# Kernel optimization log

Measured on AMD Instinct MI355X. Metric: run time of the kernel, lower is better.

Reference implementation:

```python
import jax, jax.numpy as jnp
import numpy as np

D_MODEL = 1024
NUM_HEADS = 16
HEAD_DIM = D_MODEL // NUM_HEADS


def setup_inputs() -> dict:
    key = jax.random.key(0)
    ks = jax.random.split(key, 11)
    N, S = 4, 2048
    s = 1.0 / np.sqrt(D_MODEL)
    return {
        "query": jax.random.normal(ks[0], (N, S, D_MODEL), jnp.float32),
        "key": jax.random.normal(ks[1], (N, S, D_MODEL), jnp.float32),
        "value": jax.random.normal(ks[2], (N, S, D_MODEL), jnp.float32),
        "Wq": jax.random.normal(ks[3], (D_MODEL, D_MODEL), jnp.float32) * s,
        "bq": jnp.zeros((D_MODEL,), jnp.float32),
        "Wk": jax.random.normal(ks[4], (D_MODEL, D_MODEL), jnp.float32) * s,
        "bk": jnp.zeros((D_MODEL,), jnp.float32),
        "Wv": jax.random.normal(ks[5], (D_MODEL, D_MODEL), jnp.float32) * s,
        "bv": jnp.zeros((D_MODEL,), jnp.float32),
        "Wo": jax.random.normal(ks[6], (D_MODEL, D_MODEL), jnp.float32) * s,
        "bo": jnp.zeros((D_MODEL,), jnp.float32),
    }


def reference(query, key, value, Wq, bq, Wk, bk, Wv, bv, Wo, bo):
    N, Q, _ = query.shape
    K = key.shape[1]
    # torch Linear: x @ W^T + b
    q = (query @ Wq.T + bq).reshape(N, Q, NUM_HEADS, HEAD_DIM)
    k = (key @ Wk.T + bk).reshape(N, K, NUM_HEADS, HEAD_DIM)
    v = (value @ Wv.T + bv).reshape(N, K, NUM_HEADS, HEAD_DIM)
    # NOTE: original module applies NO 1/sqrt(head_dim) scaling.
    scores = jnp.einsum('nqhd,nkhd->nhqk', q, k)
    attn = jax.nn.softmax(scores, axis=3)
    out = jnp.einsum('nhqk,nkhd->nqhd', attn, v).reshape(N, Q, D_MODEL)
    return out @ Wo.T + bo
```

## Files before the change

kernel.cpp:

```cpp
#include <hip/hip_runtime.h>
#include <stdint.h>

#define SEQ 2048
#define MROWS 8192
#define LOG2E 1.44269504f

typedef __attribute__((ext_vector_type(8))) _Float16 f16x8;
typedef __attribute__((ext_vector_type(2))) __fp16 fp16x2_t;
typedef __attribute__((ext_vector_type(8))) unsigned short ushort8;
typedef __attribute__((ext_vector_type(4))) unsigned short ushort4_t;
typedef __attribute__((ext_vector_type(4))) float f32x4;
typedef __attribute__((ext_vector_type(16))) float f32x16;

__device__ __forceinline__ unsigned short f32_to_f16u(float f) {
  union { _Float16 h; unsigned short u; } v; v.h = (_Float16)f; return v.u;
}

__device__ __forceinline__ unsigned int pk_u32(float a, float b) {
  union { fp16x2_t h; unsigned int u; } v;
  v.h = __builtin_amdgcn_cvt_pkrtz(a, b);
  return v.u;
}

__device__ __forceinline__ ushort8 pack8_rtz(float4 f0, float4 f1) {
  union { fp16x2_t h2[4]; ushort8 u8; } pk;
  pk.h2[0] = __builtin_amdgcn_cvt_pkrtz(f0.x, f0.y);
  pk.h2[1] = __builtin_amdgcn_cvt_pkrtz(f0.z, f0.w);
  pk.h2[2] = __builtin_amdgcn_cvt_pkrtz(f1.x, f1.y);
  pk.h2[3] = __builtin_amdgcn_cvt_pkrtz(f1.z, f1.w);
  return pk.u8;
}

__device__ __forceinline__ void gload16(const void* g, void* l) {
  __builtin_amdgcn_global_load_lds(
      (const __attribute__((address_space(1))) unsigned int*)g,
      (__attribute__((address_space(3))) unsigned int*)l, 16, 0, 0);
}

__global__ __launch_bounds__(256) void wconv_k(
    const float* __restrict__ Wq, const float* __restrict__ Wk,
    const float* __restrict__ Wv, const float* __restrict__ Wo,
    unsigned short* __restrict__ WF)
{
  const int plane = blockIdx.y;
  const float* __restrict__ s = (plane==0)? Wq : (plane==1)? Wk : (plane==2)? Wv : Wo;
  size_t off = ((size_t)blockIdx.x*256 + threadIdx.x) * 8;
  float4 f0 = *(const float4*)(s + off);
  float4 f1 = *(const float4*)(s + off + 4);
  *(ushort8*)&WF[(size_t)plane*1048576 + off] = pack8_rtz(f0, f1);
}

__global__ __launch_bounds__(256) void qkv_k(
    const float* __restrict__ Aq, const float* __restrict__ Ak, const float* __restrict__ Av,
    const unsigned short* __restrict__ WF,
    const float* __restrict__ bq, const float* __restrict__ bk, const float* __restrict__ bv,
    unsigned short* __restrict__ Qf, unsigned short* __restrict__ Kf, unsigned short* __restrict__ Vt)
{
  const int z = blockIdx.z;
  const float* __restrict__ A    = (z==0)? Aq : (z==1)? Ak : Av;
  const unsigned short* __restrict__ W = WF + (size_t)z*1048576;
  const float* __restrict__ bias = (z==0)? bq : (z==1)? bk : bv;

  __shared__ unsigned short Ah[128*32];
  __shared__ unsigned short Bh[128*32];

  const int tid  = threadIdx.x;
  const int lane = tid & 63;
  const int w    = tid >> 6;
  const int wm   = w >> 1, wn = w & 1;
  const int row0 = blockIdx.x * 128;
  const int col0 = blockIdx.y * 128;

  f32x4 acc[4][4] = {};

  for (int k0 = 0; k0 < 1024; k0 += 32) {
    __syncthreads();
    #pragma unroll
    for (int j=0;j<2;++j) {
      int r  = w*32 + j*16 + (lane>>2);
      int sl = (lane & 3) ^ ((r>>1)&3);
      gload16(W + (size_t)(col0 + r)*1024 + k0 + sl*8, &Bh[(w*32 + j*16)*32]);
    }
    #pragma unroll
    for (int i = 0; i < 2; ++i) {
      int c = tid + i*256;
      int r = c >> 2, slot = c & 3;
      int lidx = r*32 + ((slot ^ ((r >> 1) & 3))*8);
      const float* ap = A + (size_t)(row0 + r)*1024 + k0 + slot*8;
      float4 f0 = *(const float4*)ap;
      float4 f1 = *(const float4*)(ap + 4);
      *(ushort8*)&Ah[lidx] = pack8_rtz(f0, f1);
    }
    __syncthreads();

    f16x8 a_[4], b_[4];
    const int slotR = lane >> 4;
    #pragma unroll
    for (int m=0;m<4;++m) {
      int r = wm*64 + m*16 + (lane & 15);
      a_[m] = *(const f16x8*)&Ah[r*32 + ((slotR ^ ((r>>1)&3))*8)];
    }
    #pragma unroll
    for (int nn=0;nn<4;++nn) {
      int r = wn*64 + nn*16 + (lane & 15);
      b_[nn] = *(const f16x8*)&Bh[r*32 + ((slotR ^ ((r>>1)&3))*8)];
    }
    #pragma unroll
    for (int m=0;m<4;++m)
      #pragma unroll
      for (int nn=0;nn<4;++nn)
        acc[m][nn] = __builtin_amdgcn_mfma_f32_16x16x32_f16(a_[m], b_[nn], acc[m][nn],0,0,0);
  }

  #pragma unroll
  for (int m=0;m<4;++m) {
    #pragma unroll
    for (int nn=0;nn<4;++nn) {
      int gcol = col0 + wn*64 + nn*16 + (lane & 15);
      float bsv = bias[gcol];
      if (z == 2) {
        int rbase = row0 + wm*64 + m*16 + (lane>>4)*4;
        int nIdx = rbase >> 11, s0 = rbase & 2047;
        ushort4_t pk;
        #pragma unroll
        for (int r2=0;r2<4;++r2) pk[r2] = f32_to_f16u(acc[m][nn][r2] + bsv);
        *(ushort4_t*)&Vt[((size_t)(nIdx*1024 + gcol))*2048 + s0] = pk;
      } else {
        unsigned short* __restrict__ dst = (z==0)? Qf : Kf;
        const float qsc = (z==0)? LOG2E : 1.0f;
        #pragma unroll
        for (int r2=0;r2<4;++r2) {
          int grow = row0 + wm*64 + m*16 + (lane>>4)*4 + r2;
          dst[(size_t)grow*1024 + gcol] = f32_to_f16u((acc[m][nn][r2] + bsv) * qsc);
        }
      }
    }
  }
}

__global__ __launch_bounds__(256) void oproj_k(
    const unsigned short* __restrict__ AO, const unsigned short* __restrict__ W,
    const float* __restrict__ bias, float* __restrict__ out)
{
  __shared__ unsigned short Ah[128*32];
  __shared__ unsigned short Bh[128*32];

  const int tid  = threadIdx.x;
  const int lane = tid & 63;
  const int w    = tid >> 6;
  const int wm   = w >> 1, wn = w & 1;
  const int row0 = blockIdx.x * 128;
  const int col0 = blockIdx.y * 128;

  f32x4 acc[4][4] = {};

  for (int k0 = 0; k0 < 1024; k0 += 32) {
    __syncthreads();
    #pragma unroll
    for (int j=0;j<2;++j) {
      int r  = w*32 + j*16 + (lane>>2);
      int sl = (lane & 3) ^ ((r>>1)&3);
      gload16(AO + (size_t)(row0 + r)*1024 + k0 + sl*8, &Ah[(w*32 + j*16)*32]);
      gload16(W  + (size_t)(col0 + r)*1024 + k0 + sl*8, &Bh[(w*32 + j*16)*32]);
    }
    __syncthreads();

    f16x8 a_[4], b_[4];
    const int slotR = lane >> 4;
    #pragma unroll
    for (int m=0;m<4;++m) {
      int r = wm*64 + m*16 + (lane & 15);
      a_[m] = *(const f16x8*)&Ah[r*32 + ((slotR ^ ((r>>1)&3))*8)];
    }
    #pragma unroll
    for (int nn=0;nn<4;++nn) {
      int r = wn*64 + nn*16 + (lane & 15);
      b_[nn] = *(const f16x8*)&Bh[r*32 + ((slotR ^ ((r>>1)&3))*8)];
    }
    #pragma unroll
    for (int m=0;m<4;++m)
      #pragma unroll
      for (int nn=0;nn<4;++nn)
        acc[m][nn] = __builtin_amdgcn_mfma_f32_16x16x32_f16(a_[m], b_[nn], acc[m][nn],0,0,0);
  }

  #pragma unroll
  for (int m=0;m<4;++m)
    #pragma unroll
    for (int nn=0;nn<4;++nn) {
      int gcol = col0 + wn*64 + nn*16 + (lane & 15);
      float bsv = bias[gcol];
      #pragma unroll
      for (int r2=0;r2<4;++r2) {
        int grow = row0 + wm*64 + m*16 + (lane>>4)*4 + r2;
        out[(size_t)grow*1024 + gcol] = acc[m][nn][r2] + bsv;
      }
    }
}

__global__ __launch_bounds__(256) void attn_k(
  const unsigned short* __restrict__ Qf, const unsigned short* __restrict__ Kf,
  const unsigned short* __restrict__ Vt, unsigned short* __restrict__ AO)
{
  __shared__ unsigned short Ks[2][64*64];
  __shared__ unsigned short Vs[2][64*64];

  const int tid = threadIdx.x, lane = tid & 63, w = tid >> 6;
  const int q = lane & 31, h = lane >> 5;

  const int bid = blockIdx.x;
  const int swz = (bid & 7) * 128 + (bid >> 3);
  const int qt = swz & 15, nh = swz >> 4;
  const int n = nh >> 4, hh = nh & 15;

  f16x8 qf[4];
  {
    int qrow = n*SEQ + qt*128 + w*32 + q;
    #pragma unroll
    for (int t=0;t<4;++t)
      qf[t] = *(const f16x8*)&Qf[(size_t)qrow*1024 + hh*64 + t*16 + h*8];
  }

  f32x16 o[2] = {};
  float mrun = -1e30f, lrun = 0.f;

  const size_t kbase = (size_t)(n*SEQ)*1024 + hh*64;
  const size_t vbase = ((size_t)(n*1024 + hh*64))*SEQ;

  #pragma unroll
  for (int i=0;i<2;++i){
    int c = tid + i*256; int r = c>>3, sl = c&7;
    int lidx = r*64 + ((sl^(r&7))*8);
    *(ushort8*)&Ks[0][lidx] = *(const ushort8*)&Kf[kbase + (size_t)r*1024 + sl*8];
    *(ushort8*)&Vs[0][lidx] = *(const ushort8*)&Vt[vbase + (size_t)r*SEQ + sl*8];
  }
  __syncthreads();

  int cur = 0;
  for (int kt = 0; kt < 32; ++kt) {
    ushort8 kreg[2], vreg[2];
    if (kt < 31) {
      #pragma unroll
      for (int i=0;i<2;++i){
        int c = tid + i*256; int r = c>>3, sl = c&7;
        kreg[i] = *(const ushort8*)&Kf[kbase + (size_t)((kt+1)*64 + r)*1024 + sl*8];
        vreg[i] = *(const ushort8*)&Vt[vbase + (size_t)r*SEQ + (kt+1)*64 + sl*8];
      }
    }

    f32x16 s[2] = {};
    __builtin_amdgcn_s_setprio(1);
    #pragma unroll
    for (int t=0; t<4; ++t) {
      int gr = ((2*t+h) ^ (q&7))*8;
      f16x8 k0 = *(const f16x8*)&Ks[cur][(q     )*64 + gr];
      f16x8 k1 = *(const f16x8*)&Ks[cur][(32 + q)*64 + gr];
      s[0] = __builtin_amdgcn_mfma_f32_32x32x16_f16(k0, qf[t], s[0],0,0,0);
      s[1] = __builtin_amdgcn_mfma_f32_32x32x16_f16(k1, qf[t], s[1],0,0,0);
    }
    __builtin_amdgcn_s_setprio(0);

    float m01 = fmaxf(fmaxf(s[0][0], s[0][1]), fmaxf(s[0][2], s[0][3]));
    float m02 = fmaxf(fmaxf(s[0][4], s[0][5]), fmaxf(s[0][6], s[0][7]));
    float m03 = fmaxf(fmaxf(s[0][8], s[0][9]), fmaxf(s[0][10], s[0][11]));
    float m04 = fmaxf(fmaxf(s[0][12], s[0][13]), fmaxf(s[0][14], s[0][15]));
    float m11 = fmaxf(fmaxf(s[1][0], s[1][1]), fmaxf(s[1][2], s[1][3]));
    float m12 = fmaxf(fmaxf(s[1][4], s[1][5]), fmaxf(s[1][6], s[1][7]));
    float m13 = fmaxf(fmaxf(s[1][8], s[1][9]), fmaxf(s[1][10], s[1][11]));
    float m14 = fmaxf(fmaxf(s[1][12], s[1][13]), fmaxf(s[1][14], s[1][15]));
    float ml = fmaxf(fmaxf(fmaxf(m01,m02), fmaxf(m03,m04)),
                     fmaxf(fmaxf(m11,m12), fmaxf(m13,m14)));
    if (!__all(ml <= mrun + 7.0f)) {
      float m2 = fmaxf(ml, __shfl_xor(ml, 32, 64));
      float mn = fmaxf(mrun, m2);
      float sc = __builtin_amdgcn_exp2f(mrun - mn);
      lrun *= sc;
      mrun = mn;
      #pragma unroll
      for (int dd=0; dd<2; ++dd)
        #pragma unroll
        for (int r=0;r<16;++r) o[dd][r] *= sc;
    }
    {
      float m0 = mrun;
      float rsl = 0.f;
      #pragma unroll
      for (int st=0; st<2; ++st)
        #pragma unroll
        for (int r=0;r<16;++r) {
          float p = __builtin_amdgcn_exp2f(s[st][r] - m0);
          s[st][r] = p; rsl += p;
        }
      lrun += rsl;
    }

    f16x8 pf[4];
    #pragma unroll
    for (int st=0; st<2; ++st)
      #pragma unroll
      for (int s_t=0; s_t<2; ++s_t) {
        unsigned int a0 = pk_u32(s[st][8*s_t+0], s[st][8*s_t+1]);
        unsigned int a1 = pk_u32(s[st][8*s_t+2], s[st][8*s_t+3]);
        unsigned int b0 = pk_u32(s[st][8*s_t+4], s[st][8*s_t+5]);
        unsigned int b1 = pk_u32(s[st][8*s_t+6], s[st][8*s_t+7]);
        asm("v_permlane32_swap_b32 %0, %1" : "+v"(a0), "+v"(b0));
        asm("v_permlane32_swap_b32 %0, %1" : "+v"(a1), "+v"(b1));
        union { unsigned int u[4]; f16x8 v; } pkk;
        pkk.u[0] = a0; pkk.u[1] = a1; pkk.u[2] = b0; pkk.u[3] = b1;
        pf[st*2 + s_t] = pkk.v;
      }

    #pragma unroll
    for (int sg=0; sg<4; ++sg) {
      int gr = ((2*sg+h) ^ (q&7))*8;
      f16x8 v0 = *(const f16x8*)&Vs[cur][(q     )*64 + gr];
      f16x8 v1 = *(const f16x8*)&Vs[cur][(32 + q)*64 + gr];
      __builtin_amdgcn_s_setprio(1);
      o[0] = __builtin_amdgcn_mfma_f32_32x32x16_f16(v0, pf[sg], o[0],0,0,0);
      o[1] = __builtin_amdgcn_mfma_f32_32x32x16_f16(v1, pf[sg], o[1],0,0,0);
      __builtin_amdgcn_s_setprio(0);
    }

    if (kt < 31) {
      #pragma unroll
      for (int i=0;i<2;++i){
        int c = tid + i*256; int r = c>>3, sl = c&7;
        int lidx = r*64 + ((sl^(r&7))*8);
        *(ushort8*)&Ks[cur^1][lidx] = kreg[i];
        *(ushort8*)&Vs[cur^1][lidx] = vreg[i];
      }
    }
    __syncthreads();
    cur ^= 1;
  }

  float rs = lrun + __shfl_xor(lrun, 32, 64);
  float inv = 1.0f / rs;
  int qrow = n*SEQ + qt*128 + w*32 + q;
  #pragma unroll
  for (int dd=0; dd<2; ++dd)
    #pragma unroll
    for (int rq=0; rq<4; ++rq) {
      union { fp16x2_t h2[2]; ushort4_t u4; } pk4;
      pk4.h2[0] = __builtin_amdgcn_cvt_pkrtz(o[dd][4*rq+0]*inv, o[dd][4*rq+1]*inv);
      pk4.h2[1] = __builtin_amdgcn_cvt_pkrtz(o[dd][4*rq+2]*inv, o[dd][4*rq+3]*inv);
      int d0 = dd*32 + 8*rq + 4*h;
      *(ushort4_t*)&AO[(size_t)qrow*1024 + hh*64 + d0] = pk4.u4;
    }
}

extern "C" void kernel_launch(void* const* d_in, const int* in_sizes, int n_in,
                              void* d_out, int out_size, void* d_ws, size_t ws_size,
                              hipStream_t stream)
{
  (void)in_sizes; (void)n_in; (void)out_size; (void)ws_size;
  const float* query = (const float*)d_in[0];
  const float* key   = (const float*)d_in[1];
  const float* value = (const float*)d_in[2];
  const float* Wq = (const float*)d_in[3];
  const float* bq = (const float*)d_in[4];
  const float* Wk = (const float*)d_in[5];
  const float* bk = (const float*)d_in[6];
  const float* Wv = (const float*)d_in[7];
  const float* bv = (const float*)d_in[8];
  const float* Wo = (const float*)d_in[9];
  const float* bo = (const float*)d_in[10];
  float* out = (float*)d_out;

  unsigned short* ws = (unsigned short*)d_ws;
  const size_t PLANE = (size_t)MROWS * 1024;
  unsigned short* Qf = ws;
  unsigned short* Kf = Qf + PLANE;
  unsigned short* Vt = Kf + PLANE;
  unsigned short* AO = Vt + PLANE;
  unsigned short* WF = AO + PLANE;

  dim3 bb(256);
  wconv_k<<<dim3(512,4), bb, 0, stream>>>(Wq, Wk, Wv, Wo, WF);
  qkv_k <<<dim3(64,8,3), bb, 0, stream>>>(query,key,value, WF, bq,bk,bv, Qf,Kf,Vt);
  attn_k<<<dim3(1024), bb, 0, stream>>>(Qf, Kf, Vt, AO);
  oproj_k<<<dim3(64,8), bb, 0, stream>>>(AO, WF + 3*1048576, bo, out);
}
```

Before: 222.6 us.

## Software-pipeline attention loop so QK^T of next tile overlaps softmax of current

```diff
diff --git a/kernel.cpp b/kernel.cpp
--- a/kernel.cpp
+++ b/kernel.cpp
@@ -35,6 +35,55 @@
   __builtin_amdgcn_global_load_lds(
       (const __attribute__((address_space(1))) unsigned int*)g,
       (__attribute__((address_space(3))) unsigned int*)l, 16, 0, 0);
+}
+
+__device__ __forceinline__ void softmax32(f32x16* s, f32x16* o,
+                                          float& mrun, float& lrun, f16x8* pf) {
+  float m01 = fmaxf(fmaxf(s[0][0], s[0][1]), fmaxf(s[0][2], s[0][3]));
+  float m02 = fmaxf(fmaxf(s[0][4], s[0][5]), fmaxf(s[0][6], s[0][7]));
+  float m03 = fmaxf(fmaxf(s[0][8], s[0][9]), fmaxf(s[0][10], s[0][11]));
+  float m04 = fmaxf(fmaxf(s[0][12], s[0][13]), fmaxf(s[0][14], s[0][15]));
+  float m11 = fmaxf(fmaxf(s[1][0], s[1][1]), fmaxf(s[1][2], s[1][3]));
+  float m12 = fmaxf(fmaxf(s[1][4], s[1][5]), fmaxf(s[1][6], s[1][7]));
+  float m13 = fmaxf(fmaxf(s[1][8], s[1][9]), fmaxf(s[1][10], s[1][11]));
+  float m14 = fmaxf(fmaxf(s[1][12], s[1][13]), fmaxf(s[1][14], s[1][15]));
+  float ml = fmaxf(fmaxf(fmaxf(m01,m02), fmaxf(m03,m04)),
+                   fmaxf(fmaxf(m11,m12), fmaxf(m13,m14)));
+  if (!__all(ml <= mrun + 7.0f)) {
+    float m2 = fmaxf(ml, __shfl_xor(ml, 32, 64));
+    float mn = fmaxf(mrun, m2);
+    float sc = __builtin_amdgcn_exp2f(mrun - mn);
+    lrun *= sc;
+    mrun = mn;
+    #pragma unroll
+    for (int dd=0; dd<2; ++dd)
+      #pragma unroll
+      for (int r=0;r<16;++r) o[dd][r] *= sc;
+  }
+  float m0 = mrun;
+  float rsl = 0.f;
+  #pragma unroll
+  for (int st=0; st<2; ++st)
+    #pragma unroll
+    for (int r=0;r<16;++r) {
+      float p = __builtin_amdgcn_exp2f(s[st][r] - m0);
+      s[st][r] = p; rsl += p;
+    }
+  lrun += rsl;
+  #pragma unroll
+  for (int st=0; st<2; ++st)
+    #pragma unroll
+    for (int s_t=0; s_t<2; ++s_t) {
+      unsigned int a0 = pk_u32(s[st][8*s_t+0], s[st][8*s_t+1]);
+      unsigned int a1 = pk_u32(s[st][8*s_t+2], s[st][8*s_t+3]);
+      unsigned int b0 = pk_u32(s[st][8*s_t+4], s[st][8*s_t+5]);
+      unsigned int b1 = pk_u32(s[st][8*s_t+6], s[st][8*s_t+7]);
+      asm("v_permlane32_swap_b32 %0, %1" : "+v"(a0), "+v"(b0));
+      asm("v_permlane32_swap_b32 %0, %1" : "+v"(a1), "+v"(b1));
+      union { unsigned int u[4]; f16x8 v; } pkk;
+      pkk.u[0] = a0; pkk.u[1] = a1; pkk.u[2] = b0; pkk.u[3] = b1;
+      pf[st*2 + s_t] = pkk.v;
+    }
 }
 
 __global__ __launch_bounds__(256) void wconv_k(
@@ -222,6 +271,7 @@
   }
 
   f32x16 o[2] = {};
+  f32x16 sA[2], sB[2];
   float mrun = -1e30f, lrun = 0.f;
 
   const size_t kbase = (size_t)(n*SEQ)*1024 + hh*64;
@@ -235,104 +285,87 @@
     *(ushort8*)&Vs[0][lidx] = *(const ushort8*)&Vt[vbase + (size_t)r*SEQ + sl*8];
   }
   __syncthreads();
-
-  int cur = 0;
-  for (int kt = 0; kt < 32; ++kt) {
+  {
     ushort8 kreg[2], vreg[2];
-    if (kt < 31) {
-      #pragma unroll
-      for (int i=0;i<2;++i){
-        int c = tid + i*256; int r = c>>3, sl = c&7;
-        kreg[i] = *(const ushort8*)&Kf[kbase + (size_t)((kt+1)*64 + r)*1024 + sl*8];
-        vreg[i] = *(const ushort8*)&Vt[vbase + (size_t)r*SEQ + (kt+1)*64 + sl*8];
-      }
-    }
-
-    f32x16 s[2] = {};
+    #pragma unroll
+    for (int i=0;i<2;++i){
+      int c = tid + i*256; int r = c>>3, sl = c&7;
+      kreg[i] = *(const ushort8*)&Kf[kbase + (size_t)(64 + r)*1024 + sl*8];
+      vreg[i] = *(const ushort8*)&Vt[vbase + (size_t)r*SEQ + 64 + sl*8];
+    }
+    sA[0] = (f32x16){}; sA[1] = (f32x16){};
     __builtin_amdgcn_s_setprio(1);
     #pragma unroll
     for (int t=0; t<4; ++t) {
       int gr = ((2*t+h) ^ (q&7))*8;
-      f16x8 k0 = *(const f16x8*)&Ks[cur][(q     )*64 + gr];
-      f16x8 k1 = *(const f16x8*)&Ks[cur][(32 + q)*64 + gr];
-      s[0] = __builtin_amdgcn_mfma_f32_32x32x16_f16(k0, qf[t], s[0],0,0,0);
-      s[1] = __builtin_amdgcn_mfma_f32_32x32x16_f16(k1, qf[t], s[1],0,0,0);
+      f16x8 k0 = *(const f16x8*)&Ks[0][(q     )*64 + gr];
+      f16x8 k1 = *(const f16x8*)&Ks[0][(32 + q)*64 + gr];
+      sA[0] = __builtin_amdgcn_mfma_f32_32x32x16_f16(k0, qf[t], sA[0],0,0,0);
+      sA[1] = __builtin_amdgcn_mfma_f32_32x32x16_f16(k1, qf[t], sA[1],0,0,0);
     }
     __builtin_amdgcn_s_setprio(0);
-
-    float m01 = fmaxf(fmaxf(s[0][0], s[0][1]), fmaxf(s[0][2], s[0][3]));
-    float m02 = fmaxf(fmaxf(s[0][4], s[0][5]), fmaxf(s[0][6], s[0][7]));
-    float m03 = fmaxf(fmaxf(s[0][8], s[0][9]), fmaxf(s[0][10], s[0][11]));
-    float m04 = fmaxf(fmaxf(s[0][12], s[0][13]), fmaxf(s[0][14], s[0][15]));
-    float m11 = fmaxf(fmaxf(s[1][0], s[1][1]), fmaxf(s[1][2], s[1][3]));
-    float m12 = fmaxf(fmaxf(s[1][4], s[1][5]), fmaxf(s[1][6], s[1][7]));
-    float m13 = fmaxf(fmaxf(s[1][8], s[1][9]), fmaxf(s[1][10], s[1][11]));
-    float m14 = fmaxf(fmaxf(s[1][12], s[1][13]), fmaxf(s[1][14], s[1][15]));
-    float ml = fmaxf(fmaxf(fmaxf(m01,m02), fmaxf(m03,m04)),
-                     fmaxf(fmaxf(m11,m12), fmaxf(m13,m14)));
-    if (!__all(ml <= mrun + 7.0f)) {
-      float m2 = fmaxf(ml, __shfl_xor(ml, 32, 64));
-      float mn = fmaxf(mrun, m2);
-      float sc = __builtin_amdgcn_exp2f(mrun - mn);
-      lrun *= sc;
-      mrun = mn;
-      #pragma unroll
-      for (int dd=0; dd<2; ++dd)
-        #pragma unroll
-        for (int r=0;r<16;++r) o[dd][r] *= sc;
-    }
-    {
-      float m0 = mrun;
-      float rsl = 0.f;
-      #pragma unroll
-      for (int st=0; st<2; ++st)
-        #pragma unroll
-        for (int r=0;r<16;++r) {
-          float p = __builtin_amdgcn_exp2f(s[st][r] - m0);
-          s[st][r] = p; rsl += p;
-        }
-      lrun += rsl;
-    }
-
-    f16x8 pf[4];
-    #pragma unroll
-    for (int st=0; st<2; ++st)
-      #pragma unroll
-      for (int s_t=0; s_t<2; ++s_t) {
-        unsigned int a0 = pk_u32(s[st][8*s_t+0], s[st][8*s_t+1]);
-        unsigned int a1 = pk_u32(s[st][8*s_t+2], s[st][8*s_t+3]);
-        unsigned int b0 = pk_u32(s[st][8*s_t+4], s[st][8*s_t+5]);
-        unsigned int b1 = pk_u32(s[st][8*s_t+6], s[st][8*s_t+7]);
-        asm("v_permlane32_swap_b32 %0, %1" : "+v"(a0), "+v"(b0));
-        asm("v_permlane32_swap_b32 %0, %1" : "+v"(a1), "+v"(b1));
-        union { unsigned int u[4]; f16x8 v; } pkk;
-        pkk.u[0] = a0; pkk.u[1] = a1; pkk.u[2] = b0; pkk.u[3] = b1;
-        pf[st*2 + s_t] = pkk.v;
-      }
-
-    #pragma unroll
-    for (int sg=0; sg<4; ++sg) {
-      int gr = ((2*sg+h) ^ (q&7))*8;
-      f16x8 v0 = *(const f16x8*)&Vs[cur][(q     )*64 + gr];
-      f16x8 v1 = *(const f16x8*)&Vs[cur][(32 + q)*64 + gr];
-      __builtin_amdgcn_s_setprio(1);
-      o[0] = __builtin_amdgcn_mfma_f32_32x32x16_f16(v0, pf[sg], o[0],0,0,0);
-      o[1] = __builtin_amdgcn_mfma_f32_32x32x16_f16(v1, pf[sg], o[1],0,0,0);
-      __builtin_amdgcn_s_setprio(0);
-    }
-
-    if (kt < 31) {
-      #pragma unroll
-      for (int i=0;i<2;++i){
-        int c = tid + i*256; int r = c>>3, sl = c&7;
-        int lidx = r*64 + ((sl^(r&7))*8);
-        *(ushort8*)&Ks[cur^1][lidx] = kreg[i];
-        *(ushort8*)&Vs[cur^1][lidx] = vreg[i];
-      }
-    }
-    __syncthreads();
-    cur ^= 1;
-  }
+    #pragma unroll
+    for (int i=0;i<2;++i){
+      int c = tid + i*256; int r = c>>3, sl = c&7;
+      int lidx = r*64 + ((sl^(r&7))*8);
+      *(ushort8*)&Ks[1][lidx] = kreg[i];
+      *(ushort8*)&Vs[1][lidx] = vreg[i];
+    }
+  }
+  __syncthreads();
+
+#define ATTN_BODY(PREV, NEXT, KT, CUR)                                        \
+  {                                                                           \
+    ushort8 kreg[2], vreg[2];                                                 \
+    if ((KT) + 2 < 32) {                                                      \
+      _Pragma("unroll")                                                       \
+      for (int i=0;i<2;++i){                                                  \
+        int c = tid + i*256; int r = c>>3, sl = c&7;                          \
+        kreg[i] = *(const ushort8*)&Kf[kbase + (size_t)(((KT)+2)*64 + r)*1024 + sl*8]; \
+        vreg[i] = *(const ushort8*)&Vt[vbase + (size_t)r*SEQ + ((KT)+2)*64 + sl*8];    \
+      }                                                                       \
+    }                                                                         \
+    f16x8 pf[4];                                                              \
+    softmax32(PREV, o, mrun, lrun, pf);                                       \
+    __builtin_amdgcn_s_setprio(1);                                            \
+    _Pragma("unroll")                                                         \
+    for (int sg=0; sg<4; ++sg) {                                              \
+      int gr = ((2*sg+h) ^ (q&7))*8;                                          \
+      f16x8 v0 = *(const f16x8*)&Vs[CUR][(q     )*64 + gr];                   \
+      f16x8 v1 = *(const f16x8*)&Vs[CUR][(32 + q)*64 + gr];                   \
+      o[0] = __builtin_amdgcn_mfma_f32_32x32x16_f16(v0, pf[sg], o[0],0,0,0);  \
+      o[1] = __builtin_amdgcn_mfma_f32_32x32x16_f16(v1, pf[sg], o[1],0,0,0);  \
+    }                                                                         \
+    if ((KT) < 31) {                                                          \
+      NEXT[0] = (f32x16){}; NEXT[1] = (f32x16){};                             \
+      _Pragma("unroll")                                                       \
+      for (int t=0; t<4; ++t) {                                               \
+        int gr = ((2*t+h) ^ (q&7))*8;                                         \
+        f16x8 k0 = *(const f16x8*)&Ks[(CUR)^1][(q     )*64 + gr];             \
+        f16x8 k1 = *(const f16x8*)&Ks[(CUR)^1][(32 + q)*64 + gr];             \
+        NEXT[0] = __builtin_amdgcn_mfma_f32_32x32x16_f16(k0, qf[t], NEXT[0],0,0,0); \
+        NEXT[1] = __builtin_amdgcn_mfma_f32_32x32x16_f16(k1, qf[t], NEXT[1],0,0,0); \
+      }                                                                       \
+    }                                                                         \
+    __builtin_amdgcn_s_setprio(0);                                            \
+    __syncthreads();                                                          \
+    if ((KT) + 2 < 32) {                                                      \
+      _Pragma("unroll")                                                       \
+      for (int i=0;i<2;++i){                                                  \
+        int c = tid + i*256; int r = c>>3, sl = c&7;                          \
+        int lidx = r*64 + ((sl^(r&7))*8);                                     \
+        *(ushort8*)&Ks[CUR][lidx] = kreg[i];                                  \
+        *(ushort8*)&Vs[CUR][lidx] = vreg[i];                                  \
+      }                                                                       \
+    }                                                                         \
+    __syncthreads();                                                          \
+  }
+
+  for (int it = 0; it < 16; ++it) {
+    ATTN_BODY(sA, sB, 2*it,     0);
+    ATTN_BODY(sB, sA, 2*it + 1, 1);
+  }
+#undef ATTN_BODY
 
   float rs = lrun + __shfl_xor(lrun, 32, 64);
   float inv = 1.0f / rs;
```

Result: no change. 221.7 us (-0.4%).

## Widen attention blocks to 8 waves sharing K/V tiles, split softmax accumulators

Applied to the files above, without the earlier changes.

```diff
diff --git a/kernel.cpp b/kernel.cpp
--- a/kernel.cpp
+++ b/kernel.cpp
@@ -35,6 +35,57 @@
   __builtin_amdgcn_global_load_lds(
       (const __attribute__((address_space(1))) unsigned int*)g,
       (__attribute__((address_space(3))) unsigned int*)l, 16, 0, 0);
+}
+
+__device__ __forceinline__ void softmax32(f32x16* s, f32x16* o,
+                                          float& mrun, float& lrun, f16x8* pf) {
+  float m01 = fmaxf(fmaxf(s[0][0], s[0][1]), fmaxf(s[0][2], s[0][3]));
+  float m02 = fmaxf(fmaxf(s[0][4], s[0][5]), fmaxf(s[0][6], s[0][7]));
+  float m03 = fmaxf(fmaxf(s[0][8], s[0][9]), fmaxf(s[0][10], s[0][11]));
+  float m04 = fmaxf(fmaxf(s[0][12], s[0][13]), fmaxf(s[0][14], s[0][15]));
+  float m11 = fmaxf(fmaxf(s[1][0], s[1][1]), fmaxf(s[1][2], s[1][3]));
+  float m12 = fmaxf(fmaxf(s[1][4], s[1][5]), fmaxf(s[1][6], s[1][7]));
+  float m13 = fmaxf(fmaxf(s[1][8], s[1][9]), fmaxf(s[1][10], s[1][11]));
+  float m14 = fmaxf(fmaxf(s[1][12], s[1][13]), fmaxf(s[1][14], s[1][15]));
+  float ml = fmaxf(fmaxf(fmaxf(m01,m02), fmaxf(m03,m04)),
+                   fmaxf(fmaxf(m11,m12), fmaxf(m13,m14)));
+  if (!__all(ml <= mrun + 7.0f)) {
+    float m2 = fmaxf(ml, __shfl_xor(ml, 32, 64));
+    float mn = fmaxf(mrun, m2);
+    float sc = __builtin_amdgcn_exp2f(mrun - mn);
+    lrun *= sc;
+    mrun = mn;
+    #pragma unroll
+    for (int dd=0; dd<2; ++dd)
+      #pragma unroll
+      for (int r=0;r<16;++r) o[dd][r] *= sc;
+  }
+  float m0 = mrun;
+  float a0=0.f, a1=0.f, a2=0.f, a3=0.f;
+  #pragma unroll
+  for (int st=0; st<2; ++st)
+    #pragma unroll
+    for (int r=0;r<16;r+=4) {
+      float p0 = __builtin_amdgcn_exp2f(s[st][r+0] - m0); s[st][r+0] = p0; a0 += p0;
+      float p1 = __builtin_amdgcn_exp2f(s[st][r+1] - m0); s[st][r+1] = p1; a1 += p1;
+      float p2 = __builtin_amdgcn_exp2f(s[st][r+2] - m0); s[st][r+2] = p2; a2 += p2;
+      float p3 = __builtin_amdgcn_exp2f(s[st][r+3] - m0); s[st][r+3] = p3; a3 += p3;
+    }
+  lrun += (a0 + a1) + (a2 + a3);
+  #pragma unroll
+  for (int st=0; st<2; ++st)
+    #pragma unroll
+    for (int s_t=0; s_t<2; ++s_t) {
+      unsigned int c0 = pk_u32(s[st][8*s_t+0], s[st][8*s_t+1]);
+      unsigned int c1 = pk_u32(s[st][8*s_t+2], s[st][8*s_t+3]);
+      unsigned int d0 = pk_u32(s[st][8*s_t+4], s[st][8*s_t+5]);
+      unsigned int d1 = pk_u32(s[st][8*s_t+6], s[st][8*s_t+7]);
+      asm("v_permlane32_swap_b32 %0, %1" : "+v"(c0), "+v"(d0));
+      asm("v_permlane32_swap_b32 %0, %1" : "+v"(c1), "+v"(d1));
+      union { unsigned int u[4]; f16x8 v; } pkk;
+      pkk.u[0] = c0; pkk.u[1] = c1; pkk.u[2] = d0; pkk.u[3] = d1;
+      pf[st*2 + s_t] = pkk.v;
+    }
 }
 
 __global__ __launch_bounds__(256) void wconv_k(
@@ -198,7 +249,7 @@
     }
 }
 
-__global__ __launch_bounds__(256) void attn_k(
+__global__ __launch_bounds__(512) void attn_k(
   const unsigned short* __restrict__ Qf, const unsigned short* __restrict__ Kf,
   const unsigned short* __restrict__ Vt, unsigned short* __restrict__ AO)
 {
@@ -209,13 +260,13 @@
   const int q = lane & 31, h = lane >> 5;
 
   const int bid = blockIdx.x;
-  const int swz = (bid & 7) * 128 + (bid >> 3);
-  const int qt = swz & 15, nh = swz >> 4;
+  const int swz = (bid & 7) * 64 + (bid >> 3);
+  const int qt = swz & 7, nh = swz >> 3;
   const int n = nh >> 4, hh = nh & 15;
 
   f16x8 qf[4];
   {
-    int qrow = n*SEQ + qt*128 + w*32 + q;
+    int qrow = n*SEQ + qt*256 + w*32 + q;
     #pragma unroll
     for (int t=0;t<4;++t)
       qf[t] = *(const f16x8*)&Qf[(size_t)qrow*1024 + hh*64 + t*16 + h*8];
@@ -227,25 +278,19 @@
   const size_t kbase = (size_t)(n*SEQ)*1024 + hh*64;
   const size_t vbase = ((size_t)(n*1024 + hh*64))*SEQ;
 
-  #pragma unroll
-  for (int i=0;i<2;++i){
-    int c = tid + i*256; int r = c>>3, sl = c&7;
-    int lidx = r*64 + ((sl^(r&7))*8);
-    *(ushort8*)&Ks[0][lidx] = *(const ushort8*)&Kf[kbase + (size_t)r*1024 + sl*8];
-    *(ushort8*)&Vs[0][lidx] = *(const ushort8*)&Vt[vbase + (size_t)r*SEQ + sl*8];
-  }
+  const int sr = tid >> 3, ssl = tid & 7;
+  const int slidx = sr*64 + ((ssl^(sr&7))*8);
+
+  *(ushort8*)&Ks[0][slidx] = *(const ushort8*)&Kf[kbase + (size_t)sr*1024 + ssl*8];
+  *(ushort8*)&Vs[0][slidx] = *(const ushort8*)&Vt[vbase + (size_t)sr*SEQ + ssl*8];
   __syncthreads();
 
   int cur = 0;
   for (int kt = 0; kt < 32; ++kt) {
-    ushort8 kreg[2], vreg[2];
+    ushort8 kreg, vreg;
     if (kt < 31) {
-      #pragma unroll
-      for (int i=0;i<2;++i){
-        int c = tid + i*256; int r = c>>3, sl = c&7;
-        kreg[i] = *(const ushort8*)&Kf[kbase + (size_t)((kt+1)*64 + r)*1024 + sl*8];
-        vreg[i] = *(const ushort8*)&Vt[vbase + (size_t)r*SEQ + (kt+1)*64 + sl*8];
-      }
+      kreg = *(const ushort8*)&Kf[kbase + (size_t)((kt+1)*64 + sr)*1024 + ssl*8];
+      vreg = *(const ushort8*)&Vt[vbase + (size_t)sr*SEQ + (kt+1)*64 + ssl*8];
     }
 
     f32x16 s[2] = {};
@@ -260,55 +305,8 @@
     }
     __builtin_amdgcn_s_setprio(0);
 
-    float m01 = fmaxf(fmaxf(s[0][0], s[0][1]), fmaxf(s[0][2], s[0][3]));
-    float m02 = fmaxf(fmaxf(s[0][4], s[0][5]), fmaxf(s[0][6], s[0][7]));
-    float m03 = fmaxf(fmaxf(s[0][8], s[0][9]), fmaxf(s[0][10], s[0][11]));
-    float m04 = fmaxf(fmaxf(s[0][12], s[0][13]), fmaxf(s[0][14], s[0][15]));
-    float m11 = fmaxf(fmaxf(s[1][0], s[1][1]), fmaxf(s[1][2], s[1][3]));
-    float m12 = fmaxf(fmaxf(s[1][4], s[1][5]), fmaxf(s[1][6], s[1][7]));
-    float m13 = fmaxf(fmaxf(s[1][8], s[1][9]), fmaxf(s[1][10], s[1][11]));
-    float m14 = fmaxf(fmaxf(s[1][12], s[1][13]), fmaxf(s[1][14], s[1][15]));
-    float ml = fmaxf(fmaxf(fmaxf(m01,m02), fmaxf(m03,m04)),
-                     fmaxf(fmaxf(m11,m12), fmaxf(m13,m14)));
-    if (!__all(ml <= mrun + 7.0f)) {
-      float m2 = fmaxf(ml, __shfl_xor(ml, 32, 64));
-      float mn = fmaxf(mrun, m2);
-      float sc = __builtin_amdgcn_exp2f(mrun - mn);
-      lrun *= sc;
-      mrun = mn;
-      #pragma unroll
-      for (int dd=0; dd<2; ++dd)
-        #pragma unroll
-        for (int r=0;r<16;++r) o[dd][r] *= sc;
-    }
-    {
-      float m0 = mrun;
-      float rsl = 0.f;
-      #pragma unroll
-      for (int st=0; st<2; ++st)
-        #pragma unroll
-        for (int r=0;r<16;++r) {
-          float p = __builtin_amdgcn_exp2f(s[st][r] - m0);
-          s[st][r] = p; rsl += p;
-        }
-      lrun += rsl;
-    }
-
     f16x8 pf[4];
-    #pragma unroll
-    for (int st=0; st<2; ++st)
-      #pragma unroll
-      for (int s_t=0; s_t<2; ++s_t) {
-        unsigned int a0 = pk_u32(s[st][8*s_t+0], s[st][8*s_t+1]);
-        unsigned int a1 = pk_u32(s[st][8*s_t+2], s[st][8*s_t+3]);
-        unsigned int b0 = pk_u32(s[st][8*s_t+4], s[st][8*s_t+5]);
-        unsigned int b1 = pk_u32(s[st][8*s_t+6], s[st][8*s_t+7]);
-        asm("v_permlane32_swap_b32 %0, %1" : "+v"(a0), "+v"(b0));
-        asm("v_permlane32_swap_b32 %0, %1" : "+v"(a1), "+v"(b1));
-        union { unsigned int u[4]; f16x8 v; } pkk;
-        pkk.u[0] = a0; pkk.u[1] = a1; pkk.u[2] = b0; pkk.u[3] = b1;
-        pf[st*2 + s_t] = pkk.v;
-      }
+    softmax32(s, o, mrun, lrun, pf);
 
     #pragma unroll
     for (int sg=0; sg<4; ++sg) {
@@ -322,13 +320,8 @@
     }
 
     if (kt < 31) {
-      #pragma unroll
-      for (int i=0;i<2;++i){
-        int c = tid + i*256; int r = c>>3, sl = c&7;
-        int lidx = r*64 + ((sl^(r&7))*8);
-        *(ushort8*)&Ks[cur^1][lidx] = kreg[i];
-        *(ushort8*)&Vs[cur^1][lidx] = vreg[i];
-      }
+      *(ushort8*)&Ks[cur^1][slidx] = kreg;
+      *(ushort8*)&Vs[cur^1][slidx] = vreg;
     }
     __syncthreads();
     cur ^= 1;
@@ -336,7 +329,7 @@
 
   float rs = lrun + __shfl_xor(lrun, 32, 64);
   float inv = 1.0f / rs;
-  int qrow = n*SEQ + qt*128 + w*32 + q;
+  int qrow = n*SEQ + qt*256 + w*32 + q;
   #pragma unroll
   for (int dd=0; dd<2; ++dd)
     #pragma unroll
@@ -378,6 +371,6 @@
   dim3 bb(256);
   wconv_k<<<dim3(512,4), bb, 0, stream>>>(Wq, Wk, Wv, Wo, WF);
   qkv_k <<<dim3(64,8,3), bb, 0, stream>>>(query,key,value, WF, bq,bk,bv, Qf,Kf,Vt);
-  attn_k<<<dim3(1024), bb, 0, stream>>>(Qf, Kf, Vt, AO);
+  attn_k<<<dim3(512), dim3(512), 0, stream>>>(Qf, Kf, Vt, AO);
   oproj_k<<<dim3(64,8), bb, 0, stream>>>(AO, WF + 3*1048576, bo, out);
 }
```

Measured after the change: 208.4 us. -6.4%, faster.
